# Kernel optimization log

Hardware: AMD Instinct MI355X
Metric: run time of the kernel (lower is better)

The kernel has to match this reference:

```python
import jax, jax.numpy as jnp
import numpy as np

DEGREE = 4  # sh degree -> DEGREE**2 = 16 components
RES = 128
N_PTS = 2097152
CH = 3


def sh_components(degree, d):
    """Real SH basis values for unit directions d [..., 3] -> [..., degree**2]."""
    x, y, z = d[..., 0], d[..., 1], d[..., 2]
    xx, yy, zz = x * x, y * y, z * z
    xy, yz, xz = x * y, y * z, x * z
    comps = [jnp.full(x.shape, 0.28209479177387814, dtype=d.dtype)]
    if degree > 1:
        comps += [-0.4886025119029199 * y,
                  0.4886025119029199 * z,
                  -0.4886025119029199 * x]
    if degree > 2:
        comps += [1.0925484305920792 * xy,
                  -1.0925484305920792 * yz,
                  0.31539156525252005 * (2.0 * zz - xx - yy),
                  -1.0925484305920792 * xz,
                  0.5462742152960396 * (xx - yy)]
    if degree > 3:
        comps += [-0.5900435899266435 * y * (3 * xx - yy),
                  2.890611442640554 * xy * z,
                  -0.4570457994644658 * y * (4 * zz - xx - yy),
                  0.3731763325901154 * z * (2 * zz - 3 * xx - 3 * yy),
                  -0.4570457994644658 * x * (4 * zz - xx - yy),
                  1.445305721320277 * z * (xx - yy),
                  -0.5900435899266435 * x * (xx - 3 * yy)]
    if degree > 4:
        comps += [2.5033429417967046 * xy * (xx - yy),
                  -1.7701307697799304 * yz * (3 * xx - yy),
                  0.9461746957575601 * xy * (7 * zz - 1),
                  -0.6690465435572892 * yz * (7 * zz - 3),
                  0.10578554691520431 * (zz * (35 * zz - 30) + 3),
                  -0.6690465435572892 * xz * (7 * zz - 3),
                  0.47308734787878004 * (xx - yy) * (7 * zz - 1),
                  -1.7701307697799304 * xz * (xx - 3 * yy),
                  0.6258357354491761 * (xx * (xx - 3 * yy) - yy * (3 * xx - yy))]
    return jnp.stack(comps, axis=-1)


def trilerp(coefficients, aabb, points):
    """Trilinear interpolation of grid coefficients [R,R,R,D2,C] at points [N,3] -> [N,D2,C]."""
    res = coefficients.shape[0]
    amin, amax = aabb[:3], aabb[3:]
    g = (points - amin) / (amax - amin) * (res - 1)       # continuous grid coords
    g = jnp.clip(g, 0.0, res - 1.0)
    i0 = jnp.clip(jnp.floor(g).astype(jnp.int32), 0, res - 2)  # [N,3]
    f = g - i0.astype(g.dtype)                            # fractional part [N,3]
    fx, fy, fz = f[..., 0], f[..., 1], f[..., 2]
    out = None
    for dx in (0, 1):
        wx = fx if dx else (1.0 - fx)
        for dy in (0, 1):
            wy = fy if dy else (1.0 - fy)
            for dz in (0, 1):
                wz = fz if dz else (1.0 - fz)
                w = (wx * wy * wz)[:, None, None]          # [N,1,1]
                c = coefficients[i0[:, 0] + dx, i0[:, 1] + dy, i0[:, 2] + dz]  # [N,D2,C]
                out = w * c if out is None else out + w * c
    return out


def setup_inputs() -> dict:
    key = jax.random.key(0)
    k1, k2, k3 = jax.random.split(key, 3)
    coefficients = jax.random.normal(k1, (RES, RES, RES, DEGREE ** 2, CH), dtype=jnp.float32) * 0.1
    aabb = jnp.array([-1.0, -1.0, -1.0, 1.0, 1.0, 1.0], dtype=jnp.float32)
    points = jax.random.uniform(k2, (N_PTS, 3), dtype=jnp.float32) * 2.0 - 1.0  # inside aabb
    normals = jax.random.normal(k3, (N_PTS, 3), dtype=jnp.float32)
    normals = normals / jnp.linalg.norm(normals, axis=-1, keepdims=True)
    return {"coefficients": coefficients, "aabb": aabb, "points": points, "normals": normals}


def reference(coefficients, aabb, points, normals):
    comps = sh_components(DEGREE, normals)                 # [N, D2]
    ic = trilerp(coefficients, aabb, points)               # [N, D2, C]
    irradiance = jnp.sum(ic * comps[..., None], axis=1)    # [N, C]
    return jnp.maximum(irradiance, 0.0)
```

## Files before the change

### kernel.cpp

```cpp
#include <hip/hip_runtime.h>


constexpr int RES = 128;
constexpr int D2 = 16;
constexpr int CSTRIDE = D2 * 3;
constexpr int CELL_F4 = CSTRIDE / 4;

constexpr int NBX = 32, NBY = 16, NBZ = 16;
constexpr int NBINS = NBX * NBY * NBZ;
constexpr int HX = 5, HY = 9, HZ = 9;
constexpr int MAIN_THREADS = 256;

constexpr int SRC_COL_F4 = HZ * CELL_F4;
constexpr int COL_F4 = SRC_COL_F4 + 1;
constexpr int NCOL = HX * HY;
constexpr int TOT_SRC_F4 = NCOL * SRC_COL_F4;
constexpr int LDS_F4 = NCOL * COL_F4;
constexpr int LOAD_ITERS = (TOT_SRC_F4 + MAIN_THREADS - 1) / MAIN_THREADS;

constexpr int REPL = 4;
constexpr int CAP = 104;
constexpr int CNT_PAD = 16;
constexpr int OVF_CAP = 131072;

__device__ __forceinline__ void grid_coords(const float* aabb, float px, float py, float pz,
                                            int& ix, int& iy, int& iz,
                                            float& fx, float& fy, float& fz)
{
    const float a0 = aabb[0], a1 = aabb[1], a2 = aabb[2];
    const float b0 = aabb[3], b1 = aabb[4], b2 = aabb[5];
    float gx = (px - a0) / (b0 - a0) * (float)(RES - 1);
    float gy = (py - a1) / (b1 - a1) * (float)(RES - 1);
    float gz = (pz - a2) / (b2 - a2) * (float)(RES - 1);
    gx = fminf(fmaxf(gx, 0.0f), (float)(RES - 1));
    gy = fminf(fmaxf(gy, 0.0f), (float)(RES - 1));
    gz = fminf(fmaxf(gz, 0.0f), (float)(RES - 1));
    ix = min((int)floorf(gx), RES - 2);
    iy = min((int)floorf(gy), RES - 2);
    iz = min((int)floorf(gz), RES - 2);
    fx = gx - (float)ix;
    fy = gy - (float)iy;
    fz = gz - (float)iz;
}

__device__ __forceinline__ int bin_of(int ix, int iy, int iz)
{
    return (((ix >> 2) * NBY) + (iy >> 3)) * NBZ + (iz >> 3);
}

__device__ __forceinline__ void sh_basis(float nx, float ny, float nz, float* sh)
{
    const float xx = nx * nx, yy = ny * ny, zz = nz * nz;
    const float xy = nx * ny, yz = ny * nz, xz = nx * nz;
    sh[0]  = 0.28209479177387814f;
    sh[1]  = -0.4886025119029199f * ny;
    sh[2]  = 0.4886025119029199f * nz;
    sh[3]  = -0.4886025119029199f * nx;
    sh[4]  = 1.0925484305920792f * xy;
    sh[5]  = -1.0925484305920792f * yz;
    sh[6]  = 0.31539156525252005f * (2.0f * zz - xx - yy);
    sh[7]  = -1.0925484305920792f * xz;
    sh[8]  = 0.5462742152960396f * (xx - yy);
    sh[9]  = -0.5900435899266435f * ny * (3.0f * xx - yy);
    sh[10] = 2.890611442640554f * xy * nz;
    sh[11] = -0.4570457994644658f * ny * (4.0f * zz - xx - yy);
    sh[12] = 0.3731763325901154f * nz * (2.0f * zz - 3.0f * xx - 3.0f * yy);
    sh[13] = -0.4570457994644658f * nx * (4.0f * zz - xx - yy);
    sh[14] = 1.445305721320277f * nz * (xx - yy);
    sh[15] = -0.5900435899266435f * nx * (xx - 3.0f * yy);
}

__device__ void compute_point_global(
    const float* __restrict__ coeff,
    const float* __restrict__ aabb,
    const float* __restrict__ points,
    const float* __restrict__ normals,
    float* __restrict__ out, int i)
{
    const float px = points[3 * i + 0], py = points[3 * i + 1], pz = points[3 * i + 2];
    const float nx = normals[3 * i + 0], ny = normals[3 * i + 1], nz = normals[3 * i + 2];
    int ix, iy, iz; float fx, fy, fz;
    grid_coords(aabb, px, py, pz, ix, iy, iz, fx, fy, fz);
    float sh[D2];
    sh_basis(nx, ny, nz, sh);
    const float wz0 = 1.0f - fz, wz1 = fz;
    float acc0 = 0.0f, acc1 = 0.0f, acc2 = 0.0f;
#pragma unroll
    for (int dx = 0; dx < 2; ++dx) {
        const float wx = dx ? fx : 1.0f - fx;
#pragma unroll
        for (int dy = 0; dy < 2; ++dy) {
            const float wxy = wx * (dy ? fy : 1.0f - fy);
            const int cell = (((ix + dx) * RES + (iy + dy)) * RES + iz) * CSTRIDE;
            const float4* __restrict__ cp = (const float4*)(coeff + cell);
            union { float4 q[24]; float v[96]; } u;
#pragma unroll
            for (int kk = 0; kk < 24; ++kk) u.q[kk] = cp[kk];
            float s00 = 0.f, s01 = 0.f, s02 = 0.f;
            float s10 = 0.f, s11 = 0.f, s12 = 0.f;
#pragma unroll
            for (int j = 0; j < D2; ++j) {
                const float s = sh[j];
                s00 = fmaf(s, u.v[3 * j + 0], s00);
                s01 = fmaf(s, u.v[3 * j + 1], s01);
                s02 = fmaf(s, u.v[3 * j + 2], s02);
                s10 = fmaf(s, u.v[48 + 3 * j + 0], s10);
                s11 = fmaf(s, u.v[48 + 3 * j + 1], s11);
                s12 = fmaf(s, u.v[48 + 3 * j + 2], s12);
            }
            const float w0 = wxy * wz0, w1 = wxy * wz1;
            acc0 = fmaf(w0, s00, fmaf(w1, s10, acc0));
            acc1 = fmaf(w0, s01, fmaf(w1, s11, acc1));
            acc2 = fmaf(w0, s02, fmaf(w1, s12, acc2));
        }
    }
    out[3 * i + 0] = fmaxf(acc0, 0.0f);
    out[3 * i + 1] = fmaxf(acc1, 0.0f);
    out[3 * i + 2] = fmaxf(acc2, 0.0f);
}

__global__ __launch_bounds__(256) void scatter_kernel(
    const float* __restrict__ aabb,
    const float* __restrict__ points,
    int* __restrict__ cnt_p,
    int* __restrict__ slots,
    int* __restrict__ ovf_cnt,
    int* __restrict__ ovf,
    int n)
{
    const int i = blockIdx.x * blockDim.x + threadIdx.x;
    if (i >= n) return;
    int ix, iy, iz; float fx, fy, fz;
    grid_coords(aabb, points[3 * i + 0], points[3 * i + 1], points[3 * i + 2],
                ix, iy, iz, fx, fy, fz);
    const int bin = bin_of(ix, iy, iz);
    const int rep = (i >> 6) & (REPL - 1);
    const int g = bin * REPL + rep;
    const int pos = atomicAdd(&cnt_p[g * CNT_PAD], 1);
    if (pos < CAP) {
        slots[g * CAP + pos] = i;
    } else {
        const int o = atomicAdd(&ovf_cnt[0], 1);
        if (o < OVF_CAP) ovf[o] = i;
        else ovf_cnt[1] = 1;
    }
}

__global__ __launch_bounds__(MAIN_THREADS) void main_kernel(
    const float* __restrict__ coeff,
    const float* __restrict__ aabb,
    const float* __restrict__ points,
    const float* __restrict__ normals,
    const int* __restrict__ cnt_p,
    const int* __restrict__ slots,
    const int* __restrict__ ovf_cnt,
    const int* __restrict__ ovf,
    float* __restrict__ out,
    int n)
{
    extern __shared__ char smem[];
    float4* lds4 = (float4*)smem;

    const int bin = blockIdx.x;
    const int tid = threadIdx.x;
    const bool ovf_block = (bin == 0);

    const int c0 = min(cnt_p[(bin * REPL + 0) * CNT_PAD], CAP);
    const int c1 = min(cnt_p[(bin * REPL + 1) * CNT_PAD], CAP);
    const int c2 = min(cnt_p[(bin * REPL + 2) * CNT_PAD], CAP);
    const int c3 = min(cnt_p[(bin * REPL + 3) * CNT_PAD], CAP);
    const int tot = c0 + c1 + c2 + c3;
    if (tot == 0 && !ovf_block) return;

    if (tot > 0) {
        const int bx = bin / (NBY * NBZ);
        const int by = (bin / NBZ) % NBY;
        const int bz = bin % NBZ;
        const int x0 = bx << 2;
        const int y0 = by << 3;
        const int z0 = bz << 3;

        const float4* __restrict__ coeff4 = (const float4*)coeff;

#pragma unroll
        for (int k = 0; k < LOAD_ITERS; ++k) {
            const int u = tid + k * MAIN_THREADS;
            if (u < TOT_SRC_F4) {
                int col = u / SRC_COL_F4;
                int rem = u - col * SRC_COL_F4;
                int cx = col / HY;
                int cy = col - cx * HY;
                int cz = rem / CELL_F4;
                int kk = rem - cz * CELL_F4;
                int xg = min(x0 + cx, RES - 1);
                int yg = min(y0 + cy, RES - 1);
                int zg = min(z0 + cz, RES - 1);
                lds4[col * COL_F4 + rem] = coeff4[((xg * RES + yg) * RES + zg) * CELL_F4 + kk];
            }
        }
        __syncthreads();

        for (int t = tid; t < tot; t += MAIN_THREADS) {
            int k = t, r = 0;
            if (k >= c0) { k -= c0; r = 1;
                if (k >= c1) { k -= c1; r = 2;
                    if (k >= c2) { k -= c2; r = 3; } } }
            const int i = slots[(bin * REPL + r) * CAP + k];

            const float px = points[3 * i + 0];
            const float py = points[3 * i + 1];
            const float pz = points[3 * i + 2];
            const float nx = normals[3 * i + 0];
            const float ny = normals[3 * i + 1];
            const float nz = normals[3 * i + 2];

            int ix, iy, iz; float fx, fy, fz;
            grid_coords(aabb, px, py, pz, ix, iy, iz, fx, fy, fz);
            const int lx = ix - x0, ly = iy - y0, lz = iz - z0;

            float sh[D2];
            sh_basis(nx, ny, nz, sh);

            const float wz0 = 1.0f - fz, wz1 = fz;
            float acc0 = 0.0f, acc1 = 0.0f, acc2 = 0.0f;

#pragma unroll
            for (int dx = 0; dx < 2; ++dx) {
                const float wx = dx ? fx : 1.0f - fx;
#pragma unroll
                for (int dy = 0; dy < 2; ++dy) {
                    const float wxy = wx * (dy ? fy : 1.0f - fy);
                    const int lbase = ((lx + dx) * HY + (ly + dy)) * COL_F4 + lz * CELL_F4;
                    union { float4 q[24]; float v[96]; } u;
#pragma unroll
                    for (int kk = 0; kk < 24; ++kk) u.q[kk] = lds4[lbase + kk];

                    float s00 = 0.f, s01 = 0.f, s02 = 0.f;
                    float s10 = 0.f, s11 = 0.f, s12 = 0.f;
#pragma unroll
                    for (int j = 0; j < D2; ++j) {
                        const float s = sh[j];
                        s00 = fmaf(s, u.v[3 * j + 0], s00);
                        s01 = fmaf(s, u.v[3 * j + 1], s01);
                        s02 = fmaf(s, u.v[3 * j + 2], s02);
                        s10 = fmaf(s, u.v[48 + 3 * j + 0], s10);
                        s11 = fmaf(s, u.v[48 + 3 * j + 1], s11);
                        s12 = fmaf(s, u.v[48 + 3 * j + 2], s12);
                    }
                    const float w0 = wxy * wz0, w1 = wxy * wz1;
                    acc0 = fmaf(w0, s00, fmaf(w1, s10, acc0));
                    acc1 = fmaf(w0, s01, fmaf(w1, s11, acc1));
                    acc2 = fmaf(w0, s02, fmaf(w1, s12, acc2));
                }
            }

            out[3 * i + 0] = fmaxf(acc0, 0.0f);
            out[3 * i + 1] = fmaxf(acc1, 0.0f);
            out[3 * i + 2] = fmaxf(acc2, 0.0f);
        }
    }

    if (ovf_block) {
        const int m = min(ovf_cnt[0], OVF_CAP);
        for (int t = tid; t < m; t += MAIN_THREADS)
            compute_point_global(coeff, aabb, points, normals, out, ovf[t]);

        if (ovf_cnt[1]) {
            for (int i = tid; i < n; i += MAIN_THREADS) {
                int ix, iy, iz; float fx, fy, fz;
                grid_coords(aabb, points[3 * i + 0], points[3 * i + 1], points[3 * i + 2],
                            ix, iy, iz, fx, fy, fz);
                const int g = bin_of(ix, iy, iz) * REPL + ((i >> 6) & (REPL - 1));
                const int c = min(cnt_p[g * CNT_PAD], CAP);
                bool placed = false;
                for (int k = 0; k < c && !placed; ++k) placed = (slots[g * CAP + k] == i);
                for (int k = 0; k < m && !placed; ++k)  placed = (ovf[k] == i);
                if (!placed) compute_point_global(coeff, aabb, points, normals, out, i);
            }
        }
    }
}

__global__ __launch_bounds__(256) void direct_kernel(
    const float* __restrict__ coeff,
    const float* __restrict__ aabb,
    const float* __restrict__ points,
    const float* __restrict__ normals,
    float* __restrict__ out,
    int n)
{
    const int i = blockIdx.x * blockDim.x + threadIdx.x;
    if (i >= n) return;
    compute_point_global(coeff, aabb, points, normals, out, i);
}

extern "C" void kernel_launch(void* const* d_in, const int* in_sizes, int n_in,
                              void* d_out, int out_size, void* d_ws, size_t ws_size,
                              hipStream_t stream) {
    const float* coeff   = (const float*)d_in[0];
    const float* aabb    = (const float*)d_in[1];
    const float* points  = (const float*)d_in[2];
    const float* normals = (const float*)d_in[3];
    float* out = (float*)d_out;

    const int n = in_sizes[2] / 3;
    const int nblk = (n + 255) / 256;

    size_t off = 0;
    auto take = [&](size_t bytes) { size_t o = off; off = (off + bytes + 255) & ~(size_t)255; return o; };
    char* ws = (char*)d_ws;
    const size_t cnt_bytes = (size_t)NBINS * REPL * CNT_PAD * 4;
    const size_t o_cnt   = take(cnt_bytes);
    const size_t o_ovfc  = take(256);
    const size_t o_slots = take((size_t)NBINS * REPL * CAP * 4);
    const size_t o_ovf   = take((size_t)OVF_CAP * 4);
    const size_t needed = off;

    if (ws_size < needed) {
        hipLaunchKernelGGL(direct_kernel, dim3(nblk), dim3(256), 0, stream,
                           coeff, aabb, points, normals, out, n);
        return;
    }

    int* cnt_p   = (int*)(ws + o_cnt);
    int* ovf_cnt = (int*)(ws + o_ovfc);
    int* slots   = (int*)(ws + o_slots);
    int* ovf     = (int*)(ws + o_ovf);

    hipMemsetAsync(ws + o_cnt, 0, cnt_bytes + 256, stream);

    hipLaunchKernelGGL(scatter_kernel, dim3(nblk), dim3(256), 0, stream,
                       aabb, points, cnt_p, slots, ovf_cnt, ovf, n);
    hipLaunchKernelGGL(main_kernel, dim3(NBINS), dim3(MAIN_THREADS),
                       LDS_F4 * sizeof(float4), stream,
                       coeff, aabb, points, normals, cnt_p, slots, ovf_cnt, ovf, out, n);
}
```

Baseline: 794.8 us.

## Scatter point and normal data into binned slots instead of indices

The scatter kernel now writes each point's position, normal and index as a 32-byte record into its bin slot, so the main kernel reads them contiguously instead of gathering points and normals through an index. The memset is replaced by a small zero kernel. An index-only path is kept when the workspace is too small. This trades extra scatter write traffic and workspace for coalesced reads in the main kernel.

```diff
diff --git a/kernel.cpp b/kernel.cpp
--- a/kernel.cpp
+++ b/kernel.cpp
@@ -70,32 +70,32 @@
     sh[15] = -0.5900435899266435f * nx * (xx - 3.0f * yy);
 }
 
-__device__ void compute_point_global(
-    const float* __restrict__ coeff,
-    const float* __restrict__ aabb,
-    const float* __restrict__ points,
-    const float* __restrict__ normals,
-    float* __restrict__ out, int i)
-{
-    const float px = points[3 * i + 0], py = points[3 * i + 1], pz = points[3 * i + 2];
-    const float nx = normals[3 * i + 0], ny = normals[3 * i + 1], nz = normals[3 * i + 2];
+__device__ __forceinline__ void eval_from_lds(
+    const float4* __restrict__ lds4, const float* __restrict__ aabb,
+    float px, float py, float pz, float nx, float ny, float nz,
+    int x0, int y0, int z0, int i, float* __restrict__ out)
+{
     int ix, iy, iz; float fx, fy, fz;
     grid_coords(aabb, px, py, pz, ix, iy, iz, fx, fy, fz);
+    const int lx = ix - x0, ly = iy - y0, lz = iz - z0;
+
     float sh[D2];
     sh_basis(nx, ny, nz, sh);
+
     const float wz0 = 1.0f - fz, wz1 = fz;
     float acc0 = 0.0f, acc1 = 0.0f, acc2 = 0.0f;
+
 #pragma unroll
     for (int dx = 0; dx < 2; ++dx) {
         const float wx = dx ? fx : 1.0f - fx;
 #pragma unroll
         for (int dy = 0; dy < 2; ++dy) {
             const float wxy = wx * (dy ? fy : 1.0f - fy);
-            const int cell = (((ix + dx) * RES + (iy + dy)) * RES + iz) * CSTRIDE;
-            const float4* __restrict__ cp = (const float4*)(coeff + cell);
+            const int lbase = ((lx + dx) * HY + (ly + dy)) * COL_F4 + lz * CELL_F4;
             union { float4 q[24]; float v[96]; } u;
 #pragma unroll
-            for (int kk = 0; kk < 24; ++kk) u.q[kk] = cp[kk];
+            for (int kk = 0; kk < 24; ++kk) u.q[kk] = lds4[lbase + kk];
+
             float s00 = 0.f, s01 = 0.f, s02 = 0.f;
             float s10 = 0.f, s11 = 0.f, s12 = 0.f;
 #pragma unroll
@@ -114,12 +114,99 @@
             acc2 = fmaf(w0, s02, fmaf(w1, s12, acc2));
         }
     }
+
     out[3 * i + 0] = fmaxf(acc0, 0.0f);
     out[3 * i + 1] = fmaxf(acc1, 0.0f);
     out[3 * i + 2] = fmaxf(acc2, 0.0f);
 }
 
-__global__ __launch_bounds__(256) void scatter_kernel(
+__device__ void compute_point_global(
+    const float* __restrict__ coeff,
+    const float* __restrict__ aabb,
+    const float* __restrict__ points,
+    const float* __restrict__ normals,
+    float* __restrict__ out, int i)
+{
+    const float px = points[3 * i + 0], py = points[3 * i + 1], pz = points[3 * i + 2];
+    const float nx = normals[3 * i + 0], ny = normals[3 * i + 1], nz = normals[3 * i + 2];
+    int ix, iy, iz; float fx, fy, fz;
+    grid_coords(aabb, px, py, pz, ix, iy, iz, fx, fy, fz);
+    float sh[D2];
+    sh_basis(nx, ny, nz, sh);
+    const float wz0 = 1.0f - fz, wz1 = fz;
+    float acc0 = 0.0f, acc1 = 0.0f, acc2 = 0.0f;
+#pragma unroll
+    for (int dx = 0; dx < 2; ++dx) {
+        const float wx = dx ? fx : 1.0f - fx;
+#pragma unroll
+        for (int dy = 0; dy < 2; ++dy) {
+            const float wxy = wx * (dy ? fy : 1.0f - fy);
+            const int cell = (((ix + dx) * RES + (iy + dy)) * RES + iz) * CSTRIDE;
+            const float4* __restrict__ cp = (const float4*)(coeff + cell);
+            union { float4 q[24]; float v[96]; } u;
+#pragma unroll
+            for (int kk = 0; kk < 24; ++kk) u.q[kk] = cp[kk];
+            float s00 = 0.f, s01 = 0.f, s02 = 0.f;
+            float s10 = 0.f, s11 = 0.f, s12 = 0.f;
+#pragma unroll
+            for (int j = 0; j < D2; ++j) {
+                const float s = sh[j];
+                s00 = fmaf(s, u.v[3 * j + 0], s00);
+                s01 = fmaf(s, u.v[3 * j + 1], s01);
+                s02 = fmaf(s, u.v[3 * j + 2], s02);
+                s10 = fmaf(s, u.v[48 + 3 * j + 0], s10);
+                s11 = fmaf(s, u.v[48 + 3 * j + 1], s11);
+                s12 = fmaf(s, u.v[48 + 3 * j + 2], s12);
+            }
+            const float w0 = wxy * wz0, w1 = wxy * wz1;
+            acc0 = fmaf(w0, s00, fmaf(w1, s10, acc0));
+            acc1 = fmaf(w0, s01, fmaf(w1, s11, acc1));
+            acc2 = fmaf(w0, s02, fmaf(w1, s12, acc2));
+        }
+    }
+    out[3 * i + 0] = fmaxf(acc0, 0.0f);
+    out[3 * i + 1] = fmaxf(acc1, 0.0f);
+    out[3 * i + 2] = fmaxf(acc2, 0.0f);
+}
+
+__global__ __launch_bounds__(256) void zero_kernel(uint4* __restrict__ p, int n16)
+{
+    const int i = blockIdx.x * blockDim.x + threadIdx.x;
+    if (i < n16) p[i] = make_uint4(0u, 0u, 0u, 0u);
+}
+
+__global__ __launch_bounds__(256) void scatter_data_kernel(
+    const float* __restrict__ aabb,
+    const float* __restrict__ points,
+    const float* __restrict__ normals,
+    int* __restrict__ cnt_p,
+    float4* __restrict__ slots8,
+    int* __restrict__ ovf_cnt,
+    int* __restrict__ ovf,
+    int n)
+{
+    const int i = blockIdx.x * blockDim.x + threadIdx.x;
+    if (i >= n) return;
+    const float px = points[3 * i + 0], py = points[3 * i + 1], pz = points[3 * i + 2];
+    int ix, iy, iz; float fx, fy, fz;
+    grid_coords(aabb, px, py, pz, ix, iy, iz, fx, fy, fz);
+    const int bin = bin_of(ix, iy, iz);
+    const int rep = (i >> 6) & (REPL - 1);
+    const int g = bin * REPL + rep;
+    const int pos = atomicAdd(&cnt_p[g * CNT_PAD], 1);
+    if (pos < CAP) {
+        const float nx = normals[3 * i + 0], ny = normals[3 * i + 1], nz = normals[3 * i + 2];
+        const int rec = (g * CAP + pos) * 2;
+        slots8[rec + 0] = make_float4(px, py, pz, nx);
+        slots8[rec + 1] = make_float4(ny, nz, __int_as_float(i), 0.0f);
+    } else {
+        const int o = atomicAdd(&ovf_cnt[0], 1);
+        if (o < OVF_CAP) ovf[o] = i;
+        else ovf_cnt[1] = 1;
+    }
+}
+
+__global__ __launch_bounds__(256) void scatter_idx_kernel(
     const float* __restrict__ aabb,
     const float* __restrict__ points,
     int* __restrict__ cnt_p,
@@ -146,7 +233,100 @@
     }
 }
 
-__global__ __launch_bounds__(MAIN_THREADS) void main_kernel(
+__device__ __forceinline__ void stage_halo(
+    float4* __restrict__ lds4, const float4* __restrict__ coeff4,
+    int x0, int y0, int z0, int tid)
+{
+#pragma unroll
+    for (int k = 0; k < LOAD_ITERS; ++k) {
+        const int u = tid + k * MAIN_THREADS;
+        if (u < TOT_SRC_F4) {
+            int col = u / SRC_COL_F4;
+            int rem = u - col * SRC_COL_F4;
+            int cx = col / HY;
+            int cy = col - cx * HY;
+            int cz = rem / CELL_F4;
+            int kk = rem - cz * CELL_F4;
+            int xg = min(x0 + cx, RES - 1);
+            int yg = min(y0 + cy, RES - 1);
+            int zg = min(z0 + cz, RES - 1);
+            lds4[col * COL_F4 + rem] = coeff4[((xg * RES + yg) * RES + zg) * CELL_F4 + kk];
+        }
+    }
+}
+
+__global__ __launch_bounds__(MAIN_THREADS) void main_data_kernel(
+    const float* __restrict__ coeff,
+    const float* __restrict__ aabb,
+    const float* __restrict__ points,
+    const float* __restrict__ normals,
+    const int* __restrict__ cnt_p,
+    const float4* __restrict__ slots8,
+    const int* __restrict__ ovf_cnt,
+    const int* __restrict__ ovf,
+    float* __restrict__ out,
+    int n)
+{
+    extern __shared__ char smem[];
+    float4* lds4 = (float4*)smem;
+
+    const int bin = blockIdx.x;
+    const int tid = threadIdx.x;
+    const bool ovf_block = (bin == 0);
+
+    const int c0 = min(cnt_p[(bin * REPL + 0) * CNT_PAD], CAP);
+    const int c1 = min(cnt_p[(bin * REPL + 1) * CNT_PAD], CAP);
+    const int c2 = min(cnt_p[(bin * REPL + 2) * CNT_PAD], CAP);
+    const int c3 = min(cnt_p[(bin * REPL + 3) * CNT_PAD], CAP);
+    const int tot = c0 + c1 + c2 + c3;
+    if (tot == 0 && !ovf_block) return;
+
+    if (tot > 0) {
+        const int bx = bin / (NBY * NBZ);
+        const int by = (bin / NBZ) % NBY;
+        const int bz = bin % NBZ;
+        const int x0 = bx << 2, y0 = by << 3, z0 = bz << 3;
+
+        stage_halo(lds4, (const float4*)coeff, x0, y0, z0, tid);
+        __syncthreads();
+
+        for (int t = tid; t < tot; t += MAIN_THREADS) {
+            int k = t, r = 0;
+            if (k >= c0) { k -= c0; r = 1;
+                if (k >= c1) { k -= c1; r = 2;
+                    if (k >= c2) { k -= c2; r = 3; } } }
+            const int rec = ((bin * REPL + r) * CAP + k) * 2;
+            const float4 lo = slots8[rec + 0];
+            const float4 hi = slots8[rec + 1];
+            const int i = __float_as_int(hi.z);
+            eval_from_lds(lds4, aabb, lo.x, lo.y, lo.z, lo.w, hi.x, hi.y,
+                          x0, y0, z0, i, out);
+        }
+    }
+
+    if (ovf_block) {
+        const int m = min(ovf_cnt[0], OVF_CAP);
+        for (int t = tid; t < m; t += MAIN_THREADS)
+            compute_point_global(coeff, aabb, points, normals, out, ovf[t]);
+
+        if (ovf_cnt[1]) {
+            for (int i = tid; i < n; i += MAIN_THREADS) {
+                int ix, iy, iz; float fx, fy, fz;
+                grid_coords(aabb, points[3 * i + 0], points[3 * i + 1], points[3 * i + 2],
+                            ix, iy, iz, fx, fy, fz);
+                const int g = bin_of(ix, iy, iz) * REPL + ((i >> 6) & (REPL - 1));
+                const int c = min(cnt_p[g * CNT_PAD], CAP);
+                bool placed = false;
+                for (int k = 0; k < c && !placed; ++k)
+                    placed = (__float_as_int(slots8[(g * CAP + k) * 2 + 1].z) == i);
+                for (int k = 0; k < m && !placed; ++k) placed = (ovf[k] == i);
+                if (!placed) compute_point_global(coeff, aabb, points, normals, out, i);
+            }
+        }
+    }
+}
+
+__global__ __launch_bounds__(MAIN_THREADS) void main_idx_kernel(
     const float* __restrict__ coeff,
     const float* __restrict__ aabb,
     const float* __restrict__ points,
@@ -176,28 +356,9 @@
         const int bx = bin / (NBY * NBZ);
         const int by = (bin / NBZ) % NBY;
         const int bz = bin % NBZ;
-        const int x0 = bx << 2;
-        const int y0 = by << 3;
-        const int z0 = bz << 3;
-
-        const float4* __restrict__ coeff4 = (const float4*)coeff;
-
-#pragma unroll
-        for (int k = 0; k < LOAD_ITERS; ++k) {
-            const int u = tid + k * MAIN_THREADS;
-            if (u < TOT_SRC_F4) {
-                int col = u / SRC_COL_F4;
-                int rem = u - col * SRC_COL_F4;
-                int cx = col / HY;
-                int cy = col - cx * HY;
-                int cz = rem / CELL_F4;
-                int kk = rem - cz * CELL_F4;
-                int xg = min(x0 + cx, RES - 1);
-                int yg = min(y0 + cy, RES - 1);
-                int zg = min(z0 + cz, RES - 1);
-                lds4[col * COL_F4 + rem] = coeff4[((xg * RES + yg) * RES + zg) * CELL_F4 + kk];
-            }
-        }
+        const int x0 = bx << 2, y0 = by << 3, z0 = bz << 3;
+
+        stage_halo(lds4, (const float4*)coeff, x0, y0, z0, tid);
         __syncthreads();
 
         for (int t = tid; t < tot; t += MAIN_THREADS) {
@@ -206,57 +367,13 @@
                 if (k >= c1) { k -= c1; r = 2;
                     if (k >= c2) { k -= c2; r = 3; } } }
             const int i = slots[(bin * REPL + r) * CAP + k];
-
             const float px = points[3 * i + 0];
             const float py = points[3 * i + 1];
             const float pz = points[3 * i + 2];
             const float nx = normals[3 * i + 0];
             const float ny = normals[3 * i + 1];
             const float nz = normals[3 * i + 2];
-
-            int ix, iy, iz; float fx, fy, fz;
-            grid_coords(aabb, px, py, pz, ix, iy, iz, fx, fy, fz);
-            const int lx = ix - x0, ly = iy - y0, lz = iz - z0;
-
-            float sh[D2];
-            sh_basis(nx, ny, nz, sh);
-
-            const float wz0 = 1.0f - fz, wz1 = fz;
-            float acc0 = 0.0f, acc1 = 0.0f, acc2 = 0.0f;
-
-#pragma unroll
-            for (int dx = 0; dx < 2; ++dx) {
-                const float wx = dx ? fx : 1.0f - fx;
-#pragma unroll
-                for (int dy = 0; dy < 2; ++dy) {
-                    const float wxy = wx * (dy ? fy : 1.0f - fy);
-                    const int lbase = ((lx + dx) * HY + (ly + dy)) * COL_F4 + lz * CELL_F4;
-                    union { float4 q[24]; float v[96]; } u;
-#pragma unroll
-                    for (int kk = 0; kk < 24; ++kk) u.q[kk] = lds4[lbase + kk];
-
-                    float s00 = 0.f, s01 = 0.f, s02 = 0.f;
-                    float s10 = 0.f, s11 = 0.f, s12 = 0.f;
-#pragma unroll
-                    for (int j = 0; j < D2; ++j) {
-                        const float s = sh[j];
-                        s00 = fmaf(s, u.v[3 * j + 0], s00);
-                        s01 = fmaf(s, u.v[3 * j + 1], s01);
-                        s02 = fmaf(s, u.v[3 * j + 2], s02);
-                        s10 = fmaf(s, u.v[48 + 3 * j + 0], s10);
-                        s11 = fmaf(s, u.v[48 + 3 * j + 1], s11);
-                        s12 = fmaf(s, u.v[48 + 3 * j + 2], s12);
-                    }
-                    const float w0 = wxy * wz0, w1 = wxy * wz1;
-                    acc0 = fmaf(w0, s00, fmaf(w1, s10, acc0));
-                    acc1 = fmaf(w0, s01, fmaf(w1, s11, acc1));
-                    acc2 = fmaf(w0, s02, fmaf(w1, s12, acc2));
-                }
-            }
-
-            out[3 * i + 0] = fmaxf(acc0, 0.0f);
-            out[3 * i + 1] = fmaxf(acc1, 0.0f);
-            out[3 * i + 2] = fmaxf(acc2, 0.0f);
+            eval_from_lds(lds4, aabb, px, py, pz, nx, ny, nz, x0, y0, z0, i, out);
         }
     }
 
@@ -305,33 +422,45 @@
 
     const int n = in_sizes[2] / 3;
     const int nblk = (n + 255) / 256;
-
-    size_t off = 0;
-    auto take = [&](size_t bytes) { size_t o = off; off = (off + bytes + 255) & ~(size_t)255; return o; };
     char* ws = (char*)d_ws;
+
     const size_t cnt_bytes = (size_t)NBINS * REPL * CNT_PAD * 4;
-    const size_t o_cnt   = take(cnt_bytes);
-    const size_t o_ovfc  = take(256);
-    const size_t o_slots = take((size_t)NBINS * REPL * CAP * 4);
-    const size_t o_ovf   = take((size_t)OVF_CAP * 4);
-    const size_t needed = off;
-
-    if (ws_size < needed) {
+    const size_t ovfc_bytes = 256;
+    const size_t ovf_bytes = (size_t)OVF_CAP * 4;
+    const size_t slots_data_bytes = (size_t)NBINS * REPL * CAP * 32;
+    const size_t slots_idx_bytes  = (size_t)NBINS * REPL * CAP * 4;
+
+    const size_t need_data = cnt_bytes + ovfc_bytes + ovf_bytes + slots_data_bytes;
+    const size_t need_idx  = cnt_bytes + ovfc_bytes + ovf_bytes + slots_idx_bytes;
+
+    if (ws_size < need_idx) {
         hipLaunchKernelGGL(direct_kernel, dim3(nblk), dim3(256), 0, stream,
                            coeff, aabb, points, normals, out, n);
         return;
     }
 
-    int* cnt_p   = (int*)(ws + o_cnt);
-    int* ovf_cnt = (int*)(ws + o_ovfc);
-    int* slots   = (int*)(ws + o_slots);
-    int* ovf     = (int*)(ws + o_ovf);
-
-    hipMemsetAsync(ws + o_cnt, 0, cnt_bytes + 256, stream);
-
-    hipLaunchKernelGGL(scatter_kernel, dim3(nblk), dim3(256), 0, stream,
-                       aabb, points, cnt_p, slots, ovf_cnt, ovf, n);
-    hipLaunchKernelGGL(main_kernel, dim3(NBINS), dim3(MAIN_THREADS),
-                       LDS_F4 * sizeof(float4), stream,
-                       coeff, aabb, points, normals, cnt_p, slots, ovf_cnt, ovf, out, n);
-}
+    int* cnt_p   = (int*)(ws);
+    int* ovf_cnt = (int*)(ws + cnt_bytes);
+    int* ovf     = (int*)(ws + cnt_bytes + ovfc_bytes);
+    char* slots_base = ws + cnt_bytes + ovfc_bytes + ovf_bytes;
+
+    const int zero16 = (int)((cnt_bytes + ovfc_bytes) / 16);
+    hipLaunchKernelGGL(zero_kernel, dim3((zero16 + 255) / 256), dim3(256), 0, stream,
+                       (uint4*)ws, zero16);
+
+    if (ws_size >= need_data) {
+        float4* slots8 = (float4*)slots_base;
+        hipLaunchKernelGGL(scatter_data_kernel, dim3(nblk), dim3(256), 0, stream,
+                           aabb, points, normals, cnt_p, slots8, ovf_cnt, ovf, n);
+        hipLaunchKernelGGL(main_data_kernel, dim3(NBINS), dim3(MAIN_THREADS),
+                           LDS_F4 * sizeof(float4), stream,
+                           coeff, aabb, points, normals, cnt_p, slots8, ovf_cnt, ovf, out, n);
+    } else {
+        int* slots = (int*)slots_base;
+        hipLaunchKernelGGL(scatter_idx_kernel, dim3(nblk), dim3(256), 0, stream,
+                           aabb, points, cnt_p, slots, ovf_cnt, ovf, n);
+        hipLaunchKernelGGL(main_idx_kernel, dim3(NBINS), dim3(MAIN_THREADS),
+                           LDS_F4 * sizeof(float4), stream,
+                           coeff, aabb, points, normals, cnt_p, slots, ovf_cnt, ovf, out, n);
+    }
+}
```

Result: faster. 753.9 us (-5.1%).

## Persistent warp-specialized main kernel with double-buffered halo staging and packed point records

Applied to the files above, without the earlier changes.

The main kernel becomes persistent: each 512-thread block walks 32 consecutive bins. Half the threads evaluate points for the current bin while the other half stage the next bin's coefficient halo into a second LDS buffer, so halo loads overlap compute. The scatter pass now writes each point's position, normal and index into a 64-byte record, so the main kernel no longer gathers points and normals by index. Replication goes from 4 to 16 with smaller per-slot capacity, to reduce atomic contention. A custom zero kernel replaces the memset. The cost is double the LDS, only half the threads computing at any time, and serial bin processing within each block, which leaves only 256 blocks to fill the device.

```diff
diff --git a/kernel.cpp b/kernel.cpp
--- a/kernel.cpp
+++ b/kernel.cpp
@@ -9,17 +9,19 @@
 constexpr int NBX = 32, NBY = 16, NBZ = 16;
 constexpr int NBINS = NBX * NBY * NBZ;
 constexpr int HX = 5, HY = 9, HZ = 9;
-constexpr int MAIN_THREADS = 256;
 
 constexpr int SRC_COL_F4 = HZ * CELL_F4;
 constexpr int COL_F4 = SRC_COL_F4 + 1;
 constexpr int NCOL = HX * HY;
 constexpr int TOT_SRC_F4 = NCOL * SRC_COL_F4;
 constexpr int LDS_F4 = NCOL * COL_F4;
-constexpr int LOAD_ITERS = (TOT_SRC_F4 + MAIN_THREADS - 1) / MAIN_THREADS;
-
-constexpr int REPL = 4;
-constexpr int CAP = 104;
+
+constexpr int MAIN_THREADS = 512;
+constexpr int BINS_PER_BLOCK = 32;
+constexpr int MAIN_GRID = NBINS / BINS_PER_BLOCK;
+
+constexpr int REPL = 16;
+constexpr int CAP = 40;
 constexpr int CNT_PAD = 16;
 constexpr int OVF_CAP = 131072;
 
@@ -70,6 +72,56 @@
     sh[15] = -0.5900435899266435f * nx * (xx - 3.0f * yy);
 }
 
+__device__ __forceinline__ void eval_from_lds(
+    const float4* __restrict__ lds4, const float* __restrict__ aabb,
+    float px, float py, float pz, float nx, float ny, float nz,
+    int x0, int y0, int z0, int i, float* __restrict__ out)
+{
+    int ix, iy, iz; float fx, fy, fz;
+    grid_coords(aabb, px, py, pz, ix, iy, iz, fx, fy, fz);
+    const int lx = ix - x0, ly = iy - y0, lz = iz - z0;
+
+    float sh[D2];
+    sh_basis(nx, ny, nz, sh);
+
+    const float wz0 = 1.0f - fz, wz1 = fz;
+    float acc0 = 0.0f, acc1 = 0.0f, acc2 = 0.0f;
+
+#pragma unroll
+    for (int dx = 0; dx < 2; ++dx) {
+        const float wx = dx ? fx : 1.0f - fx;
+#pragma unroll
+        for (int dy = 0; dy < 2; ++dy) {
+            const float wxy = wx * (dy ? fy : 1.0f - fy);
+            const int lbase = ((lx + dx) * HY + (ly + dy)) * COL_F4 + lz * CELL_F4;
+            union { float4 q[24]; float v[96]; } u;
+#pragma unroll
+            for (int kk = 0; kk < 24; ++kk) u.q[kk] = lds4[lbase + kk];
+
+            float s00 = 0.f, s01 = 0.f, s02 = 0.f;
+            float s10 = 0.f, s11 = 0.f, s12 = 0.f;
+#pragma unroll
+            for (int j = 0; j < D2; ++j) {
+                const float s = sh[j];
+                s00 = fmaf(s, u.v[3 * j + 0], s00);
+                s01 = fmaf(s, u.v[3 * j + 1], s01);
+                s02 = fmaf(s, u.v[3 * j + 2], s02);
+                s10 = fmaf(s, u.v[48 + 3 * j + 0], s10);
+                s11 = fmaf(s, u.v[48 + 3 * j + 1], s11);
+                s12 = fmaf(s, u.v[48 + 3 * j + 2], s12);
+            }
+            const float w0 = wxy * wz0, w1 = wxy * wz1;
+            acc0 = fmaf(w0, s00, fmaf(w1, s10, acc0));
+            acc1 = fmaf(w0, s01, fmaf(w1, s11, acc1));
+            acc2 = fmaf(w0, s02, fmaf(w1, s12, acc2));
+        }
+    }
+
+    out[3 * i + 0] = fmaxf(acc0, 0.0f);
+    out[3 * i + 1] = fmaxf(acc1, 0.0f);
+    out[3 * i + 2] = fmaxf(acc2, 0.0f);
+}
+
 __device__ void compute_point_global(
     const float* __restrict__ coeff,
     const float* __restrict__ aabb,
@@ -119,26 +171,38 @@
     out[3 * i + 2] = fmaxf(acc2, 0.0f);
 }
 
+__global__ __launch_bounds__(256) void zero_kernel(uint4* __restrict__ p, int n16)
+{
+    for (int i = blockIdx.x * blockDim.x + threadIdx.x; i < n16; i += gridDim.x * blockDim.x)
+        p[i] = make_uint4(0u, 0u, 0u, 0u);
+}
+
 __global__ __launch_bounds__(256) void scatter_kernel(
     const float* __restrict__ aabb,
     const float* __restrict__ points,
+    const float* __restrict__ normals,
     int* __restrict__ cnt_p,
-    int* __restrict__ slots,
+    float4* __restrict__ slots4,
     int* __restrict__ ovf_cnt,
     int* __restrict__ ovf,
     int n)
 {
     const int i = blockIdx.x * blockDim.x + threadIdx.x;
     if (i >= n) return;
+    const float px = points[3 * i + 0], py = points[3 * i + 1], pz = points[3 * i + 2];
     int ix, iy, iz; float fx, fy, fz;
-    grid_coords(aabb, points[3 * i + 0], points[3 * i + 1], points[3 * i + 2],
-                ix, iy, iz, fx, fy, fz);
+    grid_coords(aabb, px, py, pz, ix, iy, iz, fx, fy, fz);
     const int bin = bin_of(ix, iy, iz);
     const int rep = (i >> 6) & (REPL - 1);
     const int g = bin * REPL + rep;
     const int pos = atomicAdd(&cnt_p[g * CNT_PAD], 1);
     if (pos < CAP) {
-        slots[g * CAP + pos] = i;
+        const float nx = normals[3 * i + 0], ny = normals[3 * i + 1], nz = normals[3 * i + 2];
+        const size_t rec = ((size_t)g * CAP + pos) * 4;
+        slots4[rec + 0] = make_float4(px, py, pz, nx);
+        slots4[rec + 1] = make_float4(ny, nz, __int_as_float(i), 0.0f);
+        slots4[rec + 2] = make_float4(0.f, 0.f, 0.f, 0.f);
+        slots4[rec + 3] = make_float4(0.f, 0.f, 0.f, 0.f);
     } else {
         const int o = atomicAdd(&ovf_cnt[0], 1);
         if (o < OVF_CAP) ovf[o] = i;
@@ -146,121 +210,110 @@
     }
 }
 
-__global__ __launch_bounds__(MAIN_THREADS) void main_kernel(
+template <int NT>
+__device__ __forceinline__ void stage_halo(
+    float4* __restrict__ dst, const float4* __restrict__ coeff4,
+    int x0, int y0, int z0, int t)
+{
+    constexpr int ITERS = (TOT_SRC_F4 + NT - 1) / NT;
+#pragma unroll
+    for (int k = 0; k < ITERS; ++k) {
+        const int u = t + k * NT;
+        if (u < TOT_SRC_F4) {
+            int col = u / SRC_COL_F4;
+            int rem = u - col * SRC_COL_F4;
+            int cx = col / HY;
+            int cy = col - cx * HY;
+            int cz = rem / CELL_F4;
+            int kk = rem - cz * CELL_F4;
+            int xg = min(x0 + cx, RES - 1);
+            int yg = min(y0 + cy, RES - 1);
+            int zg = min(z0 + cz, RES - 1);
+            dst[col * COL_F4 + rem] = coeff4[((xg * RES + yg) * RES + zg) * CELL_F4 + kk];
+        }
+    }
+}
+
+__global__ __launch_bounds__(MAIN_THREADS, 1) void main_kernel(
     const float* __restrict__ coeff,
     const float* __restrict__ aabb,
     const float* __restrict__ points,
     const float* __restrict__ normals,
     const int* __restrict__ cnt_p,
-    const int* __restrict__ slots,
+    const float4* __restrict__ slots4,
     const int* __restrict__ ovf_cnt,
     const int* __restrict__ ovf,
     float* __restrict__ out,
     int n)
 {
     extern __shared__ char smem[];
-    float4* lds4 = (float4*)smem;
-
-    const int bin = blockIdx.x;
+    float4* buf0 = (float4*)smem;
+    float4* buf1 = buf0 + LDS_F4;
+    __shared__ int s_cnt[2][REPL];
+    __shared__ int s_pref[2][REPL + 1];
+
     const int tid = threadIdx.x;
-    const bool ovf_block = (bin == 0);
-
-    const int c0 = min(cnt_p[(bin * REPL + 0) * CNT_PAD], CAP);
-    const int c1 = min(cnt_p[(bin * REPL + 1) * CNT_PAD], CAP);
-    const int c2 = min(cnt_p[(bin * REPL + 2) * CNT_PAD], CAP);
-    const int c3 = min(cnt_p[(bin * REPL + 3) * CNT_PAD], CAP);
-    const int tot = c0 + c1 + c2 + c3;
-    if (tot == 0 && !ovf_block) return;
-
-    if (tot > 0) {
-        const int bx = bin / (NBY * NBZ);
-        const int by = (bin / NBZ) % NBY;
-        const int bz = bin % NBZ;
-        const int x0 = bx << 2;
-        const int y0 = by << 3;
-        const int z0 = bz << 3;
-
-        const float4* __restrict__ coeff4 = (const float4*)coeff;
-
-#pragma unroll
-        for (int k = 0; k < LOAD_ITERS; ++k) {
-            const int u = tid + k * MAIN_THREADS;
-            if (u < TOT_SRC_F4) {
-                int col = u / SRC_COL_F4;
-                int rem = u - col * SRC_COL_F4;
-                int cx = col / HY;
-                int cy = col - cx * HY;
-                int cz = rem / CELL_F4;
-                int kk = rem - cz * CELL_F4;
-                int xg = min(x0 + cx, RES - 1);
-                int yg = min(y0 + cy, RES - 1);
-                int zg = min(z0 + cz, RES - 1);
-                lds4[col * COL_F4 + rem] = coeff4[((xg * RES + yg) * RES + zg) * CELL_F4 + kk];
+    const int bin0 = blockIdx.x * BINS_PER_BLOCK;
+    const float4* __restrict__ coeff4 = (const float4*)coeff;
+
+    {
+        const int bx = bin0 / (NBY * NBZ);
+        const int by = (bin0 / NBZ) % NBY;
+        const int bz = bin0 % NBZ;
+        stage_halo<MAIN_THREADS>(buf0, coeff4, bx << 2, by << 3, bz << 3, tid);
+        if (tid < REPL) s_cnt[0][tid] = min(cnt_p[(bin0 * REPL + tid) * CNT_PAD], CAP);
+    }
+    __syncthreads();
+    if (tid == 0) {
+        int run = 0;
+        for (int r = 0; r < REPL; ++r) { s_pref[0][r] = run; run += s_cnt[0][r]; }
+        s_pref[0][REPL] = run;
+    }
+    __syncthreads();
+
+    for (int kb = 0; kb < BINS_PER_BLOCK; ++kb) {
+        const int bin = bin0 + kb;
+        const int cur = kb & 1;
+        float4* bufc = cur ? buf1 : buf0;
+        float4* bufn = cur ? buf0 : buf1;
+
+        if (tid < 256) {
+            const int bx = bin / (NBY * NBZ);
+            const int by = (bin / NBZ) % NBY;
+            const int bz = bin % NBZ;
+            const int x0 = bx << 2, y0 = by << 3, z0 = bz << 3;
+            const int tot = s_pref[cur][REPL];
+            for (int t = tid; t < tot; t += 256) {
+                int r = 0;
+                while (r < REPL - 1 && t >= s_pref[cur][r + 1]) ++r;
+                const int k = t - s_pref[cur][r];
+                const size_t rec = ((size_t)(bin * REPL + r) * CAP + k) * 4;
+                const float4 lo = slots4[rec + 0];
+                const float4 hi = slots4[rec + 1];
+                eval_from_lds(bufc, aabb, lo.x, lo.y, lo.z, lo.w, hi.x, hi.y,
+                              x0, y0, z0, __float_as_int(hi.z), out);
+            }
+        } else if (kb + 1 < BINS_PER_BLOCK) {
+            const int nbin = bin + 1;
+            const int nbx = nbin / (NBY * NBZ);
+            const int nby = (nbin / NBZ) % NBY;
+            const int nbz = nbin % NBZ;
+            stage_halo<256>(bufn, coeff4, nbx << 2, nby << 3, nbz << 3, tid - 256);
+            if (tid >= MAIN_THREADS - REPL) {
+                const int r = tid - (MAIN_THREADS - REPL);
+                s_cnt[1 - cur][r] = min(cnt_p[(nbin * REPL + r) * CNT_PAD], CAP);
             }
         }
         __syncthreads();
-
-        for (int t = tid; t < tot; t += MAIN_THREADS) {
-            int k = t, r = 0;
-            if (k >= c0) { k -= c0; r = 1;
-                if (k >= c1) { k -= c1; r = 2;
-                    if (k >= c2) { k -= c2; r = 3; } } }
-            const int i = slots[(bin * REPL + r) * CAP + k];
-
-            const float px = points[3 * i + 0];
-            const float py = points[3 * i + 1];
-            const float pz = points[3 * i + 2];
-            const float nx = normals[3 * i + 0];
-            const float ny = normals[3 * i + 1];
-            const float nz = normals[3 * i + 2];
-
-            int ix, iy, iz; float fx, fy, fz;
-            grid_coords(aabb, px, py, pz, ix, iy, iz, fx, fy, fz);
-            const int lx = ix - x0, ly = iy - y0, lz = iz - z0;
-
-            float sh[D2];
-            sh_basis(nx, ny, nz, sh);
-
-            const float wz0 = 1.0f - fz, wz1 = fz;
-            float acc0 = 0.0f, acc1 = 0.0f, acc2 = 0.0f;
-
-#pragma unroll
-            for (int dx = 0; dx < 2; ++dx) {
-                const float wx = dx ? fx : 1.0f - fx;
-#pragma unroll
-                for (int dy = 0; dy < 2; ++dy) {
-                    const float wxy = wx * (dy ? fy : 1.0f - fy);
-                    const int lbase = ((lx + dx) * HY + (ly + dy)) * COL_F4 + lz * CELL_F4;
-                    union { float4 q[24]; float v[96]; } u;
-#pragma unroll
-                    for (int kk = 0; kk < 24; ++kk) u.q[kk] = lds4[lbase + kk];
-
-                    float s00 = 0.f, s01 = 0.f, s02 = 0.f;
-                    float s10 = 0.f, s11 = 0.f, s12 = 0.f;
-#pragma unroll
-                    for (int j = 0; j < D2; ++j) {
-                        const float s = sh[j];
-                        s00 = fmaf(s, u.v[3 * j + 0], s00);
-                        s01 = fmaf(s, u.v[3 * j + 1], s01);
-                        s02 = fmaf(s, u.v[3 * j + 2], s02);
-                        s10 = fmaf(s, u.v[48 + 3 * j + 0], s10);
-                        s11 = fmaf(s, u.v[48 + 3 * j + 1], s11);
-                        s12 = fmaf(s, u.v[48 + 3 * j + 2], s12);
-                    }
-                    const float w0 = wxy * wz0, w1 = wxy * wz1;
-                    acc0 = fmaf(w0, s00, fmaf(w1, s10, acc0));
-                    acc1 = fmaf(w0, s01, fmaf(w1, s11, acc1));
-                    acc2 = fmaf(w0, s02, fmaf(w1, s12, acc2));
-                }
-            }
-
-            out[3 * i + 0] = fmaxf(acc0, 0.0f);
-            out[3 * i + 1] = fmaxf(acc1, 0.0f);
-            out[3 * i + 2] = fmaxf(acc2, 0.0f);
-        }
-    }
-
-    if (ovf_block) {
+        if (tid == 0 && kb + 1 < BINS_PER_BLOCK) {
+            int run = 0;
+            for (int r = 0; r < REPL; ++r) { s_pref[1 - cur][r] = run; run += s_cnt[1 - cur][r]; }
+            s_pref[1 - cur][REPL] = run;
+        }
+        __syncthreads();
+    }
+
+    if (blockIdx.x == 0) {
         const int m = min(ovf_cnt[0], OVF_CAP);
         for (int t = tid; t < m; t += MAIN_THREADS)
             compute_point_global(coeff, aabb, points, normals, out, ovf[t]);
@@ -273,8 +326,9 @@
                 const int g = bin_of(ix, iy, iz) * REPL + ((i >> 6) & (REPL - 1));
                 const int c = min(cnt_p[g * CNT_PAD], CAP);
                 bool placed = false;
-                for (int k = 0; k < c && !placed; ++k) placed = (slots[g * CAP + k] == i);
-                for (int k = 0; k < m && !placed; ++k)  placed = (ovf[k] == i);
+                for (int k = 0; k < c && !placed; ++k)
+                    placed = (__float_as_int(slots4[((size_t)g * CAP + k) * 4 + 1].z) == i);
+                for (int k = 0; k < m && !placed; ++k) placed = (ovf[k] == i);
                 if (!placed) compute_point_global(coeff, aabb, points, normals, out, i);
             }
         }
@@ -305,33 +359,33 @@
 
     const int n = in_sizes[2] / 3;
     const int nblk = (n + 255) / 256;
-
-    size_t off = 0;
-    auto take = [&](size_t bytes) { size_t o = off; off = (off + bytes + 255) & ~(size_t)255; return o; };
     char* ws = (char*)d_ws;
-    const size_t cnt_bytes = (size_t)NBINS * REPL * CNT_PAD * 4;
-    const size_t o_cnt   = take(cnt_bytes);
-    const size_t o_ovfc  = take(256);
-    const size_t o_slots = take((size_t)NBINS * REPL * CAP * 4);
-    const size_t o_ovf   = take((size_t)OVF_CAP * 4);
-    const size_t needed = off;
-
-    if (ws_size < needed) {
+
+    const size_t cnt_bytes  = (size_t)NBINS * REPL * CNT_PAD * 4;
+    const size_t ovfc_bytes = 256;
+    const size_t ovf_bytes  = (size_t)OVF_CAP * 4;
+    const size_t slot_bytes = (size_t)NBINS * REPL * CAP * 64;
+    const size_t need = cnt_bytes + ovfc_bytes + ovf_bytes + slot_bytes;
+
+    if (ws_size < need) {
         hipLaunchKernelGGL(direct_kernel, dim3(nblk), dim3(256), 0, stream,
                            coeff, aabb, points, normals, out, n);
         return;
     }
 
-    int* cnt_p   = (int*)(ws + o_cnt);
-    int* ovf_cnt = (int*)(ws + o_ovfc);
-    int* slots   = (int*)(ws + o_slots);
-    int* ovf     = (int*)(ws + o_ovf);
-
-    hipMemsetAsync(ws + o_cnt, 0, cnt_bytes + 256, stream);
+    int*    cnt_p   = (int*)(ws);
+    int*    ovf_cnt = (int*)(ws + cnt_bytes);
+    int*    ovf     = (int*)(ws + cnt_bytes + ovfc_bytes);
+    float4* slots4  = (float4*)(ws + cnt_bytes + ovfc_bytes + ovf_bytes);
+
+    const int zero16 = (int)((cnt_bytes + ovfc_bytes) / 16);
+    hipLaunchKernelGGL(zero_kernel, dim3(2048), dim3(256), 0, stream,
+                       (uint4*)ws, zero16);
 
     hipLaunchKernelGGL(scatter_kernel, dim3(nblk), dim3(256), 0, stream,
-                       aabb, points, cnt_p, slots, ovf_cnt, ovf, n);
-    hipLaunchKernelGGL(main_kernel, dim3(NBINS), dim3(MAIN_THREADS),
-                       LDS_F4 * sizeof(float4), stream,
-                       coeff, aabb, points, normals, cnt_p, slots, ovf_cnt, ovf, out, n);
-}
+                       aabb, points, normals, cnt_p, slots4, ovf_cnt, ovf, n);
+
+    hipLaunchKernelGGL(main_kernel, dim3(MAIN_GRID), dim3(MAIN_THREADS),
+                       2 * LDS_F4 * sizeof(float4), stream,
+                       coeff, aabb, points, normals, cnt_p, slots4, ovf_cnt, ovf, out, n);
+}
```

Result: slower. 811.5 us (+2.1%).
